# Performance work log

Measured on AMD Instinct MI355X. Metric: run time of the kernel, lower is better.

The kernel has to match this reference:

```python
import jax, jax.numpy as jnp
import numpy as np
from jax import lax

B, C, H, W = 16, 3, 256, 256
K = 3          # lbp kernel size (odd)
POOL = 2
Q = 8          # quant_len
LN_EPS = 1e-5


def _lbp_kernel(c, k):
    half = k // 2
    idx_pairs = [[[0, 0], [k - 1, k - 1]],
                 [[0, half], [k - 1, half]],
                 [[0, k - 1], [k - 1, 0]],
                 [[half, k - 1], [half, 0]]]
    kerns = []
    for pair in idx_pairs:
        for idx in pair:
            m = np.zeros((c, k, k), np.float32)
            m[:, half, half] = 1.0
            m[:, idx[0], idx[1]] = -1.0
            kerns.append(m)
    return jnp.asarray(np.stack(kerns))  # [8, C, K, K]


LBP_KERNEL = _lbp_kernel(C, K)


def setup_inputs() -> dict:
    key = jax.random.key(0)
    ks = jax.random.split(key, 8)
    return {
        "x": jax.random.normal(ks[0], (B, C, H, W), jnp.float32),
        "clamp_low": jnp.float32(-150.0),
        "clamp_high": jnp.float32(150.0),
        "w_expand": jax.random.normal(ks[1], (56, 3, 1, 1), jnp.float32) * 0.1,
        "b_expand": jax.random.normal(ks[2], (56,), jnp.float32) * 0.05,
        "w_conv": jax.random.normal(ks[3], (16, 4, 1, 1), jnp.float32) * 0.1,
        "b_conv": jax.random.normal(ks[4], (16,), jnp.float32) * 0.05,
        "w_final": jax.random.normal(ks[5], (1, 16, 3, 3), jnp.float32) * 0.1,
        "b_final": jax.random.normal(ks[6], (1,), jnp.float32) * 0.05,
    }


def reference(x, clamp_low, clamp_high, w_expand, b_expand, w_conv, b_conv, w_final, b_final):
    leaky = lambda v: jax.nn.leaky_relu(v, 0.01)
    bsz = x.shape[0]

    # avg_pool2d(kernel=POOL, stride=1, pad=POOL//2, count_include_pad=True) -> [B,C,H+1,W+1]
    pad = POOL // 2
    xp = lax.reduce_window(x, 0.0, lax.add, (1, 1, POOL, POOL), (1, 1, 1, 1),
                           [(0, 0), (0, 0), (pad, pad), (pad, pad)]) / float(POOL * POOL)

    # LBP difference conv: 8 output channels, SAME padding
    hk = K // 2
    xl = lax.conv_general_dilated(xp, LBP_KERNEL, (1, 1), [(hk, hk), (hk, hk)],
                                  dimension_numbers=("NCHW", "OIHW", "NCHW"))
    xl = jnp.clip(xl, clamp_low, clamp_high)

    b4 = bsz * 4
    hp, wp = xl.shape[-2], xl.shape[-1]
    n = hp * wp
    xl = xl.reshape(b4, 2, n)  # [B4, 2, N]

    # per-sample, per-channel quantization boundaries: measure[b,i,c] = i*cd + min
    mn = xl.min(axis=-1)                       # [B4, 2]
    mx = xl.max(axis=-1)                       # [B4, 2]
    cd = (mx - mn) / Q
    measure = jnp.arange(Q + 1, dtype=xl.dtype)[None, :, None] * cd[:, None, :] + mn[:, None, :]  # [B4,Q+1,2]

    def bin_mask(vals, ch):
        # keep raw value where lo_i <= v <= hi_i, else 0  -> [B4, Q, N]
        v = vals[:, None, :]
        lo = measure[:, :-1, ch][:, :, None]
        hi = measure[:, 1:, ch][:, :, None]
        return jnp.where((v >= lo) & (v <= hi), v, 0.0)

    m0 = bin_mask(xl[:, 0, :], 0)  # [B4, Q, N]
    m1 = bin_mask(xl[:, 1, :], 1)  # [B4, Q, N]

    # joint histogram of masked values: equivalent to per-pixel outer product + one-hot mask conv
    hist = jnp.einsum("bin,bjn->bij", m0, m1)       # [B4, Q, Q]
    hist = hist / jnp.sum(hist)                      # global normalizer (torch.sum(x))
    hist = hist.reshape(b4, Q * Q, 1)

    # levels: (bin_index + 1) * measure[:, 1, :]
    ii, jj = jnp.meshgrid(jnp.arange(Q), jnp.arange(Q), indexing="ij")
    idxs = jnp.stack([ii, jj], axis=-1).reshape(Q * Q, 2)          # cartesian_prod order
    levels = (idxs[None].astype(xl.dtype) + 1.0) * measure[:, 1, :][:, None, :]  # [B4,64,2]

    feat = jnp.concatenate([levels, hist], axis=2)   # [B4, 64, 3]
    feat = feat.reshape(bsz, 4, Q * Q, 3).transpose(0, 3, 1, 2)  # [B, 3, 4, 64]

    # 1x1 conv 3 -> 56
    h = leaky(jnp.einsum("bcij,oc->boij", feat, w_expand[:, :, 0, 0]) + b_expand[None, :, None, None])
    h = h.transpose(0, 2, 3, 1)  # [B, 4, 64, 56] -> channels=4, spatial (64,56)

    # nearest interpolate spatial (64,56) -> (H,W): src = floor(dst * in / out)
    src_h = (jnp.arange(H) * h.shape[2]) // H
    src_w = (jnp.arange(W) * h.shape[3]) // W
    h = h[:, :, src_h][:, :, :, src_w]  # [B, 4, H, W]

    # layer_norm over last two dims, no affine
    mean = h.mean(axis=(-2, -1), keepdims=True)
    var = jnp.mean((h - mean) ** 2, axis=(-2, -1), keepdims=True)
    h = (h - mean) / jnp.sqrt(var + LN_EPS)

    # 1x1 conv 4 -> 16
    h = leaky(jnp.einsum("bchw,oc->bohw", h, w_conv[:, :, 0, 0]) + b_conv[None, :, None, None])

    # 3x3 conv 16 -> 1, SAME padding
    out = lax.conv_general_dilated(h, w_final, (1, 1), [(1, 1), (1, 1)],
                                   dimension_numbers=("NCHW", "OIHW", "NCHW"))
    out = leaky(out + b_final[None, :, None, None])
    return out
```

## Files before the change

kernel.cpp:

```cpp
#include <hip/hip_runtime.h>
#include <stdint.h>
#include <math.h>

#define HH 256
#define WW 256
#define BATCH 16
#define HP 257
#define SROW 264
#define SH 259
#define SBP (SH*SROW)
#define NPIX (HP*HP)
#define TS 32
#define TH 9
#define NT (TH*TH)

__device__ __forceinline__ float leaky(float v){ return v >= 0.f ? v : 0.01f*v; }

__device__ __forceinline__ void group_off(int k, int& dh, int& dw){
    dh = (k == 3) ? 0 : -1;
    dw = (k == 3) ? 1 : (k - 1);
}

__global__ __launch_bounds__(256) void k12(const float* __restrict__ x, float* __restrict__ s,
                                           float* __restrict__ pmn, float* __restrict__ pmx,
                                           float* __restrict__ hist){
    __shared__ float xs[35][36];
    __shared__ float sh[34][35];
    __shared__ float redmn[4][8], redmx[4][8];
    int blk = blockIdx.x, tid = threadIdx.x;
    int wv = tid >> 6, lane = tid & 63;
    int b = blk / NT, tile = blk % NT;
    int ty = tile / TH, tx = tile % TH;

    if (blk == 0){
        for (int t = tid; t < 4096; t += 256) hist[t] = 0.f;
    }
    if (blk < BATCH){
        float* sb = s + (size_t)blk*SBP;
        for (int t = tid; t < 2*SROW; t += 256){
            int rr = (t < SROW) ? 0 : 258; int cc = t % SROW;
            sb[rr*SROW + cc] = 0.f;
        }
        for (int t = tid; t < 257*7; t += 256){
            int rr = 1 + t/7, k = t%7;
            int cc = (k == 0) ? 0 : (257 + k);
            sb[rr*SROW + cc] = 0.f;
        }
    }

    const float* xb = x + (size_t)b*3*HH*WW;
    int xr0 = ty*TS - 2, xc0 = tx*TS - 2;
    for (int t = tid; t < 35*35; t += 256){
        int i = t/35, j = t - i*35;
        int r = xr0 + i, c = xc0 + j;
        float v = 0.f;
        if ((unsigned)r < (unsigned)HH && (unsigned)c < (unsigned)WW){
            int o = r*WW + c;
            v = xb[o] + xb[HH*WW + o] + xb[2*HH*WW + o];
        }
        xs[i][j] = v;
    }
    __syncthreads();

    for (int t = tid; t < 34*34; t += 256){
        int i = t/34, j = t - i*34;
        int h = ty*TS - 1 + i, w = tx*TS - 1 + j;
        float v = 0.f;
        if ((unsigned)h < (unsigned)HP && (unsigned)w < (unsigned)HP)
            v = 0.25f*(xs[i][j] + xs[i][j+1] + xs[i+1][j] + xs[i+1][j+1]);
        sh[i][j] = v;
    }
    __syncthreads();

    float mn[8], mx[8];
    #pragma unroll
    for (int q=0;q<8;q++){ mn[q]=INFINITY; mx[q]=-INFINITY; }
    float* sb = s + (size_t)b*SBP;
    #pragma unroll
    for (int q4=0; q4<4; ++q4){
        int p = q4*256 + tid;
        int lr = p >> 5, lc = p & 31;
        int h = ty*TS + lr, w = tx*TS + lc;
        if (h < HP && w < HP){
            float c = sh[lr+1][lc+1];
            sb[(h+1)*SROW + (w+1)] = c;
            float d;
            d = c - sh[lr  ][lc  ]; mn[0]=fminf(mn[0],d); mx[0]=fmaxf(mx[0],d);
            d = c - sh[lr+2][lc+2]; mn[1]=fminf(mn[1],d); mx[1]=fmaxf(mx[1],d);
            d = c - sh[lr  ][lc+1]; mn[2]=fminf(mn[2],d); mx[2]=fmaxf(mx[2],d);
            d = c - sh[lr+2][lc+1]; mn[3]=fminf(mn[3],d); mx[3]=fmaxf(mx[3],d);
            d = c - sh[lr  ][lc+2]; mn[4]=fminf(mn[4],d); mx[4]=fmaxf(mx[4],d);
            d = c - sh[lr+2][lc  ]; mn[5]=fminf(mn[5],d); mx[5]=fmaxf(mx[5],d);
            d = c - sh[lr+1][lc+2]; mn[6]=fminf(mn[6],d); mx[6]=fmaxf(mx[6],d);
            d = c - sh[lr+1][lc  ]; mn[7]=fminf(mn[7],d); mx[7]=fmaxf(mx[7],d);
        }
    }
    #pragma unroll
    for (int off=32; off; off>>=1){
        #pragma unroll
        for (int q=0;q<8;q++){
            mn[q] = fminf(mn[q], __shfl_down(mn[q], off));
            mx[q] = fmaxf(mx[q], __shfl_down(mx[q], off));
        }
    }
    if (lane == 0){
        #pragma unroll
        for (int q=0;q<8;q++){ redmn[wv][q]=mn[q]; redmx[wv][q]=mx[q]; }
    }
    __syncthreads();
    if (tid < 8){
        pmn[(size_t)blk*8 + tid] = fminf(fminf(redmn[0][tid],redmn[1][tid]),
                                         fminf(redmn[2][tid],redmn[3][tid]));
        pmx[(size_t)blk*8 + tid] = fmaxf(fmaxf(redmx[0][tid],redmx[1][tid]),
                                         fmaxf(redmx[2][tid],redmx[3][tid]));
    }
}

__global__ __launch_bounds__(256) void k3_hist(const float* __restrict__ s, const float* __restrict__ cl,
                                               const float* __restrict__ chp,
                                               const float* __restrict__ pmn, const float* __restrict__ pmx,
                                               float* __restrict__ hist){
    __shared__ float lh[4*64*32];
    int b = blockIdx.y;
    int wv = threadIdx.x >> 6, lane = threadIdx.x & 63;
    for (int t = threadIdx.x; t < 4*64*32; t += 256) lh[t] = 0.f;

    float mnA=INFINITY, mxA=-INFINITY, mnB=INFINITY, mxB=-INFINITY;
    for (int t = lane; t < NT; t += 64){
        const float* pn = pmn + ((size_t)(b*NT + t))*8;
        const float* px = pmx + ((size_t)(b*NT + t))*8;
        mnA = fminf(mnA, pn[2*wv]);   mxA = fmaxf(mxA, px[2*wv]);
        mnB = fminf(mnB, pn[2*wv+1]); mxB = fmaxf(mxB, px[2*wv+1]);
    }
    #pragma unroll
    for (int off=32; off; off>>=1){
        mnA = fminf(mnA, __shfl_down(mnA, off)); mxA = fmaxf(mxA, __shfl_down(mxA, off));
        mnB = fminf(mnB, __shfl_down(mnB, off)); mxB = fmaxf(mxB, __shfl_down(mxB, off));
    }
    mnA = __shfl(mnA, 0); mxA = __shfl(mxA, 0);
    mnB = __shfl(mnB, 0); mxB = __shfl(mxB, 0);
    float lo = cl[0], hi = chp[0];
    float mn0 = fminf(fmaxf(mnA, lo), hi), mx0 = fminf(fmaxf(mxA, lo), hi);
    float mn1 = fminf(fmaxf(mnB, lo), hi), mx1 = fminf(fmaxf(mxB, lo), hi);
    float cd0 = (mx0-mn0)*0.125f;
    float cd1 = (mx1-mn1)*0.125f;
    float m0[9], m1[9];
    #pragma unroll
    for (int i=0;i<9;i++){
        m0[i] = __fadd_rn(__fmul_rn((float)i, cd0), mn0);
        m1[i] = __fadd_rn(__fmul_rn((float)i, cd1), mn1);
    }
    int g = b*4 + wv;
    int dh, dw; group_off(wv, dh, dw);
    int doff = dh*SROW + dw;
    const float* sp = s + (size_t)b*SBP + SROW + 1;
    float* lhg = lh + wv*2048 + (lane & 31);
    __syncthreads();
    for (int idx = blockIdx.x*64 + lane; idx < NPIX; idx += 32*64){
        int h = idx / HP, w = idx - h*HP;
        const float* p = sp + h*SROW + w;
        float c = p[0];
        float v0 = fminf(fmaxf(c - p[doff],  lo), hi);
        float v1 = fminf(fmaxf(c - p[-doff], lo), hi);
        unsigned b0=0, b1=0;
        #pragma unroll
        for (int i=0;i<8;i++){
            b0 |= (v0>=m0[i] && v0<=m0[i+1]) ? (1u<<i) : 0u;
            b1 |= (v1>=m1[i] && v1<=m1[i+1]) ? (1u<<i) : 0u;
        }
        float pr = v0*v1;
        unsigned bb0=b0;
        while (bb0){
            int i = __ffs(bb0)-1; bb0 &= bb0-1;
            unsigned bb1=b1;
            while (bb1){
                int j = __ffs(bb1)-1; bb1 &= bb1-1;
                atomicAdd(&lhg[(i*8+j)*32], pr);
            }
        }
    }
    __syncthreads();
    float acc = 0.f;
    #pragma unroll
    for (int r=0;r<32;r++) acc += lh[(wv*64 + lane)*32 + ((lane + r)&31)];
    atomicAdd(&hist[g*64 + lane], acc);
}

__global__ __launch_bounds__(256) void k45(const float* __restrict__ hist,
                    const float* __restrict__ pmn, const float* __restrict__ pmx,
                    const float* __restrict__ cl, const float* __restrict__ chp,
                    const float* __restrict__ we, const float* __restrict__ be,
                    const float* __restrict__ wc, const float* __restrict__ bc,
                    const float* __restrict__ wf,
                    float* __restrict__ w9g){
    __shared__ float hloc[4*3584];
    __shared__ float wfl[144];
    __shared__ float wred[4][16];
    __shared__ float gmn[8], gmx[8];
    __shared__ float gstat[8];
    __shared__ float sred[4];
    int b = blockIdx.x, tid = threadIdx.x;
    int wv = tid >> 6, lane = tid & 63;
    if (tid < 144) wfl[tid] = wf[tid];

    float rmn[8], rmx[8];
    #pragma unroll
    for (int q=0;q<8;q++){ rmn[q]=INFINITY; rmx[q]=-INFINITY; }
    for (int t = tid; t < NT; t += 256){
        const float* pn = pmn + ((size_t)(b*NT + t))*8;
        const float* px = pmx + ((size_t)(b*NT + t))*8;
        #pragma unroll
        for (int q=0;q<8;q++){ rmn[q]=fminf(rmn[q],pn[q]); rmx[q]=fmaxf(rmx[q],px[q]); }
    }
    #pragma unroll
    for (int off=32; off; off>>=1){
        #pragma unroll
        for (int q=0;q<8;q++){
            rmn[q] = fminf(rmn[q], __shfl_down(rmn[q], off));
            rmx[q] = fmaxf(rmx[q], __shfl_down(rmx[q], off));
        }
    }
    if (lane == 0){
        #pragma unroll
        for (int q=0;q<8;q++){ wred[wv][q]=rmn[q]; wred[wv][8+q]=rmx[q]; }
    }
    __syncthreads();
    if (tid < 8)
        gmn[tid] = fminf(fminf(wred[0][tid],wred[1][tid]), fminf(wred[2][tid],wred[3][tid]));
    else if (tid < 16){
        int q = tid-8;
        gmx[q] = fmaxf(fmaxf(wred[0][8+q],wred[1][8+q]), fmaxf(wred[2][8+q],wred[3][8+q]));
    }

    float ps = 0.f;
    for (int t = tid; t < 4096; t += 256) ps += hist[t];
    #pragma unroll
    for (int off=32; off; off>>=1) ps += __shfl_down(ps, off);
    if (lane == 0) sred[wv] = ps;
    __syncthreads();
    float S = sred[0]+sred[1]+sred[2]+sred[3];

    int g = b*4 + wv;
    float lo = cl[0], hi = chp[0];
    float mn0 = fminf(fmaxf(gmn[2*wv  ], lo), hi), mx0 = fminf(fmaxf(gmx[2*wv  ], lo), hi);
    float mn1 = fminf(fmaxf(gmn[2*wv+1], lo), hi), mx1 = fminf(fmaxf(gmx[2*wv+1], lo), hi);
    float lvl0 = __fadd_rn(__fmul_rn(1.0f,(mx0-mn0)*0.125f), mn0);
    float lvl1 = __fadd_rn(__fmul_rn(1.0f,(mx1-mn1)*0.125f), mn1);
    for (int e = lane; e < 3584; e += 64){
        int ij = e/56, o = e - ij*56;
        int i = ij>>3, j = ij&7;
        float f0 = __fmul_rn((float)(i+1), lvl0);
        float f1 = __fmul_rn((float)(j+1), lvl1);
        float f2 = hist[g*64+ij] / S;
        float a = f0*we[o*3+0] + f1*we[o*3+1] + f2*we[o*3+2] + be[o];
        hloc[wv*3584 + e] = leaky(a);
    }
    float pm = 0.f;
    for (int e = lane; e < 3584; e += 64){
        int o = e%56;
        int lo_ = (32*o+6)/7, hi_ = (32*o+31)/7;
        pm += hloc[wv*3584+e] * (float)(4*(hi_-lo_+1));
    }
    #pragma unroll
    for (int off=32; off; off>>=1) pm += __shfl_down(pm, off);
    pm = __shfl(pm, 0);
    float mean = pm * (1.0f/65536.0f);
    float pv = 0.f;
    for (int e = lane; e < 3584; e += 64){
        int o = e%56;
        int lo_ = (32*o+6)/7, hi_ = (32*o+31)/7;
        float d = hloc[wv*3584+e] - mean;
        pv += d*d * (float)(4*(hi_-lo_+1));
    }
    #pragma unroll
    for (int off=32; off; off>>=1) pv += __shfl_down(pv, off);
    pv = __shfl(pv, 0);
    if (lane == 0){
        gstat[wv*2+0] = mean;
        gstat[wv*2+1] = 1.0f / sqrtf(pv * (1.0f/65536.0f) + 1e-5f);
    }
    __syncthreads();

    for (int e = tid; e < 3584; e += 256){
        float hn[4];
        #pragma unroll
        for (int k=0;k<4;k++) hn[k] = (hloc[k*3584+e] - gstat[2*k]) * gstat[2*k+1];
        float w9v[9] = {0,0,0,0,0,0,0,0,0};
        #pragma unroll
        for (int c=0;c<16;c++){
            float hv = bc[c];
            #pragma unroll
            for (int k=0;k<4;k++) hv += wc[c*4+k]*hn[k];
            hv = leaky(hv);
            #pragma unroll
            for (int t=0;t<9;t++) w9v[t] += wfl[c*9+t]*hv;
        }
        int r = e/56, sxc = e - r*56;
        float* dst = w9g + (((size_t)b*64 + r)*9)*56 + sxc;
        #pragma unroll
        for (int t=0;t<9;t++) dst[t*56] = w9v[t];
    }
}

__global__ __launch_bounds__(256) void k5_out(const float* __restrict__ w9g, const float* __restrict__ bf,
                                              float* __restrict__ out){
    int x = threadIdx.x;
    int y = blockIdx.x & 255;
    int b = blockIdx.x >> 8;
    const float* wb = w9g + (size_t)b*64*9*56;
    float acc = bf[0];
    int sxm = ((x-1)*7) >> 5;
    int sx0 = (x*7) >> 5;
    int sxp = ((x+1)*7) >> 5;
    #pragma unroll
    for (int dy=0; dy<3; ++dy){
        int yy = y + dy - 1;
        if ((unsigned)yy >= 256u) continue;
        const float* wr = wb + (((yy>>2)*9) + dy*3)*56;
        if (x >= 1)   acc += wr[0*56 + sxm];
                      acc += wr[1*56 + sx0];
        if (x <= 254) acc += wr[2*56 + sxp];
    }
    out[((size_t)(b*256 + y))*256 + x] = leaky(acc);
}

extern "C" void kernel_launch(void* const* d_in, const int* in_sizes, int n_in,
                              void* d_out, int out_size, void* d_ws, size_t ws_size,
                              hipStream_t stream){
    const float* x  = (const float*)d_in[0];
    const float* cl = (const float*)d_in[1];
    const float* ch = (const float*)d_in[2];
    const float* we = (const float*)d_in[3];
    const float* be = (const float*)d_in[4];
    const float* wc = (const float*)d_in[5];
    const float* bc = (const float*)d_in[6];
    const float* wf = (const float*)d_in[7];
    const float* bf = (const float*)d_in[8];
    float* out = (float*)d_out;

    float* s = (float*)d_ws;
    size_t off = (size_t)BATCH*SBP;
    float* pmn  = s + off; off += (size_t)BATCH*NT*8;
    float* pmx  = s + off; off += (size_t)BATCH*NT*8;
    float* hist = s + off; off += 4096;
    float* w9g  = s + off; off += (size_t)16*64*9*56;

    k12<<<BATCH*NT, 256, 0, stream>>>(x, s, pmn, pmx, hist);
    k3_hist<<<dim3(32,BATCH), 256, 0, stream>>>(s, cl, ch, pmn, pmx, hist);
    k45<<<BATCH, 256, 0, stream>>>(hist, pmn, pmx, cl, ch, we, be, wc, bc, wf, w9g);
    k5_out<<<16*256, 256, 0, stream>>>(w9g, bf, out);
}
```

Before: 156.3 us.

## Stage row bands in LDS for histogram and fuse head into output kernel

```diff
diff --git a/kernel.cpp b/kernel.cpp
--- a/kernel.cpp
+++ b/kernel.cpp
@@ -121,9 +121,21 @@
                                                const float* __restrict__ pmn, const float* __restrict__ pmx,
                                                float* __restrict__ hist){
     __shared__ float lh[4*64*32];
-    int b = blockIdx.y;
-    int wv = threadIdx.x >> 6, lane = threadIdx.x & 63;
-    for (int t = threadIdx.x; t < 4*64*32; t += 256) lh[t] = 0.f;
+    __shared__ float band[7][260];
+    int bx = blockIdx.x, b = blockIdx.y;
+    int tid = threadIdx.x;
+    int wv = tid >> 6, lane = tid & 63;
+    int h0 = bx*4;
+    int nr = (bx == 63) ? 5 : 4;
+
+    for (int t = tid; t < 4*64*32; t += 256) lh[t] = 0.f;
+
+    const float* sb = s + (size_t)b*SBP;
+    int total = (nr+2)*259;
+    for (int t = tid; t < total; t += 256){
+        int lr = t/259, wc = t - lr*259;
+        band[lr][wc] = sb[(size_t)(h0+lr)*SROW + wc];
+    }
 
     float mnA=INFINITY, mxA=-INFINITY, mnB=INFINITY, mxB=-INFINITY;
     for (int t = lane; t < NT; t += 64){
@@ -152,16 +164,16 @@
     }
     int g = b*4 + wv;
     int dh, dw; group_off(wv, dh, dw);
-    int doff = dh*SROW + dw;
-    const float* sp = s + (size_t)b*SBP + SROW + 1;
     float* lhg = lh + wv*2048 + (lane & 31);
     __syncthreads();
-    for (int idx = blockIdx.x*64 + lane; idx < NPIX; idx += 32*64){
-        int h = idx / HP, w = idx - h*HP;
-        const float* p = sp + h*SROW + w;
-        float c = p[0];
-        float v0 = fminf(fmaxf(c - p[doff],  lo), hi);
-        float v1 = fminf(fmaxf(c - p[-doff], lo), hi);
+
+    int npx = nr*257;
+    for (int p = lane; p < npx; p += 64){
+        int lrr = p/257;
+        int w = p - lrr*257;
+        float c = band[lrr+1][w+1];
+        float v0 = fminf(fmaxf(c - band[lrr+1+dh][w+1+dw], lo), hi);
+        float v1 = fminf(fmaxf(c - band[lrr+1-dh][w+1-dw], lo), hi);
         unsigned b0=0, b1=0;
         #pragma unroll
         for (int i=0;i<8;i++){
@@ -183,23 +195,25 @@
     float acc = 0.f;
     #pragma unroll
     for (int r=0;r<32;r++) acc += lh[(wv*64 + lane)*32 + ((lane + r)&31)];
-    atomicAdd(&hist[g*64 + lane], acc);
-}
-
-__global__ __launch_bounds__(256) void k45(const float* __restrict__ hist,
+    if (acc != 0.f) atomicAdd(&hist[g*64 + lane], acc);
+}
+
+__global__ __launch_bounds__(256) void k45f(const float* __restrict__ hist,
                     const float* __restrict__ pmn, const float* __restrict__ pmx,
                     const float* __restrict__ cl, const float* __restrict__ chp,
                     const float* __restrict__ we, const float* __restrict__ be,
                     const float* __restrict__ wc, const float* __restrict__ bc,
-                    const float* __restrict__ wf,
-                    float* __restrict__ w9g){
+                    const float* __restrict__ wf, const float* __restrict__ bf,
+                    float* __restrict__ out){
     __shared__ float hloc[4*3584];
+    __shared__ float w9l[4*9*56];
     __shared__ float wfl[144];
     __shared__ float wred[4][16];
     __shared__ float gmn[8], gmx[8];
     __shared__ float gstat[8];
     __shared__ float sred[4];
-    int b = blockIdx.x, tid = threadIdx.x;
+    int ch = blockIdx.x, b = blockIdx.y;
+    int tid = threadIdx.x;
     int wv = tid >> 6, lane = tid & 63;
     if (tid < 144) wfl[tid] = wf[tid];
 
@@ -281,10 +295,15 @@
     }
     __syncthreads();
 
-    for (int e = tid; e < 3584; e += 256){
+    int rm = (2*ch-1 > 0) ? (2*ch-1) : 0;
+    int rp = (2*ch+2 < 63) ? (2*ch+2) : 63;
+    int ne = (rp-rm+1)*56;
+    for (int e = tid; e < ne; e += 256){
+        int rr = e/56, sxc = e - rr*56;
+        int eg = (rm+rr)*56 + sxc;
         float hn[4];
         #pragma unroll
-        for (int k=0;k<4;k++) hn[k] = (hloc[k*3584+e] - gstat[2*k]) * gstat[2*k+1];
+        for (int k=0;k<4;k++) hn[k] = (hloc[k*3584+eg] - gstat[2*k]) * gstat[2*k+1];
         float w9v[9] = {0,0,0,0,0,0,0,0,0};
         #pragma unroll
         for (int c=0;c<16;c++){
@@ -295,33 +314,30 @@
             #pragma unroll
             for (int t=0;t<9;t++) w9v[t] += wfl[c*9+t]*hv;
         }
-        int r = e/56, sxc = e - r*56;
-        float* dst = w9g + (((size_t)b*64 + r)*9)*56 + sxc;
-        #pragma unroll
-        for (int t=0;t<9;t++) dst[t*56] = w9v[t];
-    }
-}
-
-__global__ __launch_bounds__(256) void k5_out(const float* __restrict__ w9g, const float* __restrict__ bf,
-                                              float* __restrict__ out){
-    int x = threadIdx.x;
-    int y = blockIdx.x & 255;
-    int b = blockIdx.x >> 8;
-    const float* wb = w9g + (size_t)b*64*9*56;
-    float acc = bf[0];
+        #pragma unroll
+        for (int t=0;t<9;t++) w9l[rr*504 + t*56 + sxc] = w9v[t];
+    }
+    __syncthreads();
+
+    float bf0 = bf[0];
+    int x = tid;
     int sxm = ((x-1)*7) >> 5;
     int sx0 = (x*7) >> 5;
     int sxp = ((x+1)*7) >> 5;
-    #pragma unroll
-    for (int dy=0; dy<3; ++dy){
-        int yy = y + dy - 1;
-        if ((unsigned)yy >= 256u) continue;
-        const float* wr = wb + (((yy>>2)*9) + dy*3)*56;
-        if (x >= 1)   acc += wr[0*56 + sxm];
-                      acc += wr[1*56 + sx0];
-        if (x <= 254) acc += wr[2*56 + sxp];
-    }
-    out[((size_t)(b*256 + y))*256 + x] = leaky(acc);
+    for (int yo=0; yo<8; ++yo){
+        int y = ch*8 + yo;
+        float acc = bf0;
+        #pragma unroll
+        for (int dy=0; dy<3; ++dy){
+            int yy = y + dy - 1;
+            if ((unsigned)yy >= 256u) continue;
+            const float* wr = &w9l[((yy>>2) - rm)*504 + dy*3*56];
+            if (x >= 1)   acc += wr[sxm];
+                          acc += wr[56 + sx0];
+            if (x <= 254) acc += wr[2*56 + sxp];
+        }
+        out[((size_t)(b*256 + y))*256 + x] = leaky(acc);
+    }
 }
 
 extern "C" void kernel_launch(void* const* d_in, const int* in_sizes, int n_in,
@@ -343,10 +359,8 @@
     float* pmn  = s + off; off += (size_t)BATCH*NT*8;
     float* pmx  = s + off; off += (size_t)BATCH*NT*8;
     float* hist = s + off; off += 4096;
-    float* w9g  = s + off; off += (size_t)16*64*9*56;
 
     k12<<<BATCH*NT, 256, 0, stream>>>(x, s, pmn, pmx, hist);
-    k3_hist<<<dim3(32,BATCH), 256, 0, stream>>>(s, cl, ch, pmn, pmx, hist);
-    k45<<<BATCH, 256, 0, stream>>>(hist, pmn, pmx, cl, ch, we, be, wc, bc, wf, w9g);
-    k5_out<<<16*256, 256, 0, stream>>>(w9g, bf, out);
-}
+    k3_hist<<<dim3(64,BATCH), 256, 0, stream>>>(s, cl, ch, pmn, pmx, hist);
+    k45f<<<dim3(32,BATCH), 256, 0, stream>>>(hist, pmn, pmx, cl, ch, we, be, wc, bc, wf, bf, out);
+}
```

After: 158.5 us. About the same (+1.4%).
